# Optimization experiments

Measured on AMD Instinct MI355X. Metric: run time of the kernel, lower is better.

## Reference

```python
import jax, jax.numpy as jnp
import numpy as np
import math

D_RES, N_HEADS, D_HEAD, D_MLP = 1024, 16, 64, 4096
EPS = 1e-5
IGNORE = -100000.0


def setup_inputs() -> dict:
    key = jax.random.key(0)
    ks = jax.random.split(key, 8)
    std = 0.02
    return {
        "resid_pre": jax.random.normal(ks[0], (2, 2048, D_RES), dtype=jnp.float32),
        "ln1_w": jnp.ones((D_RES,), jnp.float32),
        "ln1_b": jnp.zeros((D_RES,), jnp.float32),
        "W_Q": jax.random.normal(ks[1], (N_HEADS, D_RES, D_HEAD), jnp.float32) * std,
        "b_Q": jnp.zeros((N_HEADS, D_HEAD), jnp.float32),
        "W_K": jax.random.normal(ks[2], (N_HEADS, D_RES, D_HEAD), jnp.float32) * std,
        "b_K": jnp.zeros((N_HEADS, D_HEAD), jnp.float32),
        "W_V": jax.random.normal(ks[3], (N_HEADS, D_RES, D_HEAD), jnp.float32) * std,
        "b_V": jnp.zeros((N_HEADS, D_HEAD), jnp.float32),
        "W_O": jax.random.normal(ks[4], (N_HEADS, D_HEAD, D_RES), jnp.float32) * std,
        "b_O": jnp.zeros((D_RES,), jnp.float32),
        "ln2_w": jnp.ones((D_RES,), jnp.float32),
        "ln2_b": jnp.zeros((D_RES,), jnp.float32),
        "W_in": jax.random.normal(ks[5], (D_RES, D_MLP), jnp.float32) * std,
        "b_in": jnp.zeros((D_MLP,), jnp.float32),
        "W_out": jax.random.normal(ks[6], (D_MLP, D_RES), jnp.float32) * std,
        "b_out": jnp.zeros((D_RES,), jnp.float32),
    }


def _layernorm(x, w, b):
    x = x - jnp.mean(x, axis=-1, keepdims=True)
    scale = jnp.sqrt(jnp.mean(x * x, axis=-1, keepdims=True) + EPS)
    return (x / scale) * w + b


def reference(resid_pre, ln1_w, ln1_b, W_Q, b_Q, W_K, b_K, W_V, b_V, W_O, b_O,
              ln2_w, ln2_b, W_in, b_in, W_out, b_out):
    x = _layernorm(resid_pre, ln1_w, ln1_b)  # [b,s,d]
    q = jnp.einsum('bsd,hde->bshe', x, W_Q) + b_Q
    k = jnp.einsum('bsd,hde->bshe', x, W_K) + b_K
    v = jnp.einsum('bsd,hde->bshe', x, W_V) + b_V
    scores = jnp.einsum('bqhe,bkhe->bhqk', q, k) / math.sqrt(D_HEAD)
    S = scores.shape[-1]
    mask = jnp.triu(jnp.ones((S, S), dtype=bool), k=1)
    scores = jnp.where(mask, IGNORE, scores)
    pattern = jax.nn.softmax(scores, axis=-1)
    z = jnp.einsum('bhqk,bkhe->bqhe', pattern, v)
    attn_out = jnp.einsum('bqhe,hed->bqd', z, W_O) + b_O
    resid_mid = resid_pre + attn_out
    y = _layernorm(resid_mid, ln2_w, ln2_b)
    pre = jnp.einsum('bsd,dm->bsm', y, W_in) + b_in
    post = jax.nn.gelu(pre, approximate=False)
    mlp_out = jnp.einsum('bsm,md->bsd', post, W_out) + b_out
    return resid_mid + mlp_out
```

## Files before the change

kernel.cpp:

```cpp
#include <hip/hip_runtime.h>
#include <cstddef>

typedef unsigned short u16;
using short8 = __attribute__((ext_vector_type(8))) short;
using f32x4  = __attribute__((ext_vector_type(4))) float;

__device__ __forceinline__ float bf2f(u16 u) {
  union { unsigned int i; float f; } v; v.i = ((unsigned int)u) << 16; return v.f;
}
__device__ __forceinline__ u16 f2bf(float f) {
  __bf16 h = (__bf16)f;
  return __builtin_bit_cast(unsigned short, h);
}

__device__ __forceinline__ void load_lds16(const u16* g, u16* l) {
  __builtin_amdgcn_global_load_lds((const __attribute__((address_space(1))) void*)g,
                                   (__attribute__((address_space(3))) void*)l, 16, 0, 0);
}

__global__ __launch_bounds__(256) void transpose_k(const float* __restrict__ in,
                                                   u16* __restrict__ out,
                                                   int R, int C,
                                                   long inB, long outB) {
  __shared__ float tile[32][33];
  long zb = blockIdx.z;
  in  += zb * inB;
  out += zb * outB;
  int c0 = blockIdx.x * 32, r0 = blockIdx.y * 32;
  int tx = threadIdx.x, ty = threadIdx.y;
#pragma unroll
  for (int i = 0; i < 32; i += 8)
    tile[ty + i][tx] = in[(long)(r0 + ty + i) * C + c0 + tx];
  __syncthreads();
#pragma unroll
  for (int i = 0; i < 32; i += 8)
    out[(long)(c0 + ty + i) * R + r0 + tx] = f2bf(tile[tx][ty + i]);
}

__global__ __launch_bounds__(256) void transpose_v_k(const u16* __restrict__ qkv,
                                                     u16* __restrict__ vT) {
  __shared__ u16 tile[32][33];
  int bh = blockIdx.z;
  int b = bh >> 4, h = bh & 15;
  const u16* in = qkv + (size_t)b * 2048 * 3072 + 2048 + h * 64;
  u16* out = vT + (size_t)bh * 64 * 2048;
  int e0 = blockIdx.x * 32, s0 = blockIdx.y * 32;
  int tx = threadIdx.x, ty = threadIdx.y;
#pragma unroll
  for (int i = 0; i < 32; i += 8)
    tile[ty + i][tx] = in[(size_t)(s0 + ty + i) * 3072 + e0 + tx];
  __syncthreads();
#pragma unroll
  for (int i = 0; i < 32; i += 8)
    out[(size_t)(e0 + ty + i) * 2048 + s0 + tx] = tile[tx][ty + i];
}

__global__ void build_qkv_bias(const float* __restrict__ bQ, const float* __restrict__ bK,
                               const float* __restrict__ bV, float* __restrict__ out) {
  int i = blockIdx.x * 256 + threadIdx.x;
  float v;
  if (i < 1024) v = bQ[i];
  else if (i < 2048) v = bK[i - 1024];
  else v = bV[i - 2048];
  out[i] = v;
}

__global__ __launch_bounds__(256) void ln_k(const float* __restrict__ inp,
                                            const float* __restrict__ w,
                                            const float* __restrict__ bias,
                                            u16* __restrict__ out) {
  __shared__ float red[2][4];
  int row = blockIdx.x, t = threadIdx.x;
  int wave = t >> 6, lane = t & 63;
  size_t base = (size_t)row * 1024 + t * 4;
  float4 f = *(const float4*)(inp + base);
  float v[4] = {f.x, f.y, f.z, f.w};
  float s = v[0] + v[1] + v[2] + v[3];
#pragma unroll
  for (int off = 32; off; off >>= 1) s += __shfl_xor(s, off, 64);
  if (lane == 0) red[0][wave] = s;
  __syncthreads();
  float mean = (red[0][0] + red[0][1] + red[0][2] + red[0][3]) * (1.f / 1024.f);
  float c[4]; float sq = 0.f;
#pragma unroll
  for (int j = 0; j < 4; ++j) { c[j] = v[j] - mean; sq += c[j] * c[j]; }
#pragma unroll
  for (int off = 32; off; off >>= 1) sq += __shfl_xor(sq, off, 64);
  if (lane == 0) red[1][wave] = sq;
  __syncthreads();
  float var = (red[1][0] + red[1][1] + red[1][2] + red[1][3]) * (1.f / 1024.f);
  float inv = 1.f / sqrtf(var + 1e-5f);
  float4 wv = *(const float4*)(w + t * 4);
  float4 bv = *(const float4*)(bias + t * 4);
  out[base + 0] = f2bf(c[0] * inv * wv.x + bv.x);
  out[base + 1] = f2bf(c[1] * inv * wv.y + bv.y);
  out[base + 2] = f2bf(c[2] * inv * wv.z + bv.z);
  out[base + 3] = f2bf(c[3] * inv * wv.w + bv.w);
}

template<int TN, bool RESIDF, bool GELU, bool OUTF32>
__global__ __launch_bounds__(256, 2) void gemm_k(const u16* __restrict__ A,
                                                 const u16* __restrict__ BT,
                                                 const float* __restrict__ bias,
                                                 const float* __restrict__ resid,
                                                 void* __restrict__ Cout,
                                                 int M, int N, int K) {
  constexpr int NS = TN / 32;
  __shared__ u16 As[128 * 64];
  __shared__ u16 Bs[TN * 64];
  int n0 = blockIdx.x * TN, m0 = blockIdx.y * 128;
  int t = threadIdx.x;
  int wave = t >> 6, lane = t & 63;
  int wr = wave >> 1, wc = wave & 1;
  int ln16 = lane & 15, quad = lane >> 4;

  f32x4 acc[4][NS];
#pragma unroll
  for (int i = 0; i < 4; ++i)
#pragma unroll
    for (int j = 0; j < NS; ++j) acc[i][j] = (f32x4){0.f, 0.f, 0.f, 0.f};

  int lrow8 = lane >> 3;
  int gseg  = (lane & 7) ^ lrow8;
  const u16* aG = A  + (size_t)(m0 + wave * 8 + lrow8) * K + gseg * 8;
  const u16* bG = BT + (size_t)(n0 + wave * 8 + lrow8) * K + gseg * 8;
  u16* aL = As + wave * 8 * 64;
  u16* bL = Bs + wave * 8 * 64;

  int e = ln16 & 7;
  int arow = wr * 64 + ln16;
  int brow = wc * (TN / 2) + ln16;

  for (int k0 = 0; k0 < K; k0 += 64) {
    __syncthreads();
#pragma unroll
    for (int i = 0; i < 4; ++i)
      load_lds16(aG + (size_t)i * 32 * K + k0, aL + i * 32 * 64);
#pragma unroll
    for (int i = 0; i < TN / 32; ++i)
      load_lds16(bG + (size_t)i * 32 * K + k0, bL + i * 32 * 64);
    __syncthreads();
#pragma unroll
    for (int kk = 0; kk < 2; ++kk) {
      int slot = (kk * 4 + quad) ^ e;
      short8 af[4], bf[NS];
#pragma unroll
      for (int ms = 0; ms < 4; ++ms)
        af[ms] = *(const short8*)&As[(arow + ms * 16) * 64 + slot * 8];
#pragma unroll
      for (int ns = 0; ns < NS; ++ns)
        bf[ns] = *(const short8*)&Bs[(brow + ns * 16) * 64 + slot * 8];
#pragma unroll
      for (int ms = 0; ms < 4; ++ms)
#pragma unroll
        for (int ns = 0; ns < NS; ++ns)
          acc[ms][ns] = __builtin_amdgcn_mfma_f32_16x16x32_bf16(af[ms], bf[ns], acc[ms][ns], 0, 0, 0);
    }
  }

#pragma unroll
  for (int ms = 0; ms < 4; ++ms)
#pragma unroll
    for (int ns = 0; ns < NS; ++ns)
#pragma unroll
      for (int r = 0; r < 4; ++r) {
        int grow = m0 + wr * 64 + ms * 16 + quad * 4 + r;
        int gcol = n0 + wc * (TN / 2) + ns * 16 + ln16;
        size_t idx = (size_t)grow * N + gcol;
        float v = acc[ms][ns][r] + bias[gcol];
        if (GELU) v = 0.5f * v * (1.f + erff(v * 0.70710678118654752f));
        if (RESIDF) v += resid[idx];
        if (OUTF32) ((float*)Cout)[idx] = v;
        else        ((u16*)Cout)[idx] = f2bf(v);
      }
}

template<bool GELU>
__global__ __launch_bounds__(512, 2) void gemm256_k(const u16* __restrict__ A,
                                                    const u16* __restrict__ BT,
                                                    const float* __restrict__ bias,
                                                    u16* __restrict__ C,
                                                    int M, int N, int K) {
  constexpr int SLOT = 8192;
  __shared__ __align__(16) u16 As[4 * SLOT];
  __shared__ __align__(16) u16 Bs[4 * SLOT];
  int n0 = blockIdx.x * 256, m0 = blockIdx.y * 256;
  int t = threadIdx.x;
  int w = t >> 6, lane = t & 63;
  int wr = w >> 2, wc = w & 3;
  int ln16 = lane & 15, quad = lane >> 4;

  f32x4 acc[8][4];
#pragma unroll
  for (int i = 0; i < 8; ++i)
#pragma unroll
    for (int j = 0; j < 4; ++j) acc[i][j] = (f32x4){0.f, 0.f, 0.f, 0.f};

  const u16* aG0 = A  + (size_t)(m0 + w * 32 + (lane >> 2)) * K + (lane & 3) * 8;
  const u16* bG0 = BT + (size_t)(n0 + w * 32 + (lane >> 2)) * K + (lane & 3) * 8;
  u16* aL0 = As + w * 1024;
  u16* bL0 = Bs + w * 1024;

#define STAGE_A(j, tg) do {                                         \
    const u16* _g = aG0 + (size_t)(j) * 32;                         \
    u16* _l = aL0 + (tg) * SLOT;                                    \
    load_lds16(_g, _l);                                             \
    load_lds16(_g + (size_t)16 * K, _l + 512);                      \
  } while (0)
#define STAGE_B(j, tg) do {                                         \
    const u16* _g = bG0 + (size_t)(j) * 32;                         \
    u16* _l = bL0 + (tg) * SLOT;                                    \
    load_lds16(_g, _l);                                             \
    load_lds16(_g + (size_t)16 * K, _l + 512);                      \
  } while (0)

  STAGE_A(0, 0); STAGE_B(0, 0);
  STAGE_A(1, 1); STAGE_B(1, 1);
  STAGE_A(2, 2); STAGE_B(2, 2);
  asm volatile("s_waitcnt vmcnt(8)" ::: "memory");
  __builtin_amdgcn_s_barrier();

  int nslot = K >> 5;
  const u16* aRd = As + (wr * 128 + ln16) * 32 + quad * 8;
  const u16* bRd = Bs + (wc * 64  + ln16) * 32 + quad * 8;

  for (int s = 0; s < nslot; ++s) {
    int cur = s & 3, tgt = (s + 3) & 3;
    const u16* aB = aRd + cur * SLOT;
    const u16* bB = bRd + cur * SLOT;
    short8 a[4], b[4];

#pragma unroll
    for (int i = 0; i < 4; ++i) a[i] = *(const short8*)(aB + i * 512);
#pragma unroll
    for (int i = 0; i < 4; ++i) b[i] = *(const short8*)(bB + i * 512);
    if (s + 3 < nslot) STAGE_A(s + 3, tgt);
    __builtin_amdgcn_s_barrier();
    __builtin_amdgcn_s_setprio(1);
#pragma unroll
    for (int ms = 0; ms < 4; ++ms)
#pragma unroll
      for (int ns = 0; ns < 4; ++ns)
        acc[ms][ns] = __builtin_amdgcn_mfma_f32_16x16x32_bf16(a[ms], b[ns], acc[ms][ns], 0, 0, 0);
    __builtin_amdgcn_s_setprio(0);
    __builtin_amdgcn_s_barrier();

#pragma unroll
    for (int i = 0; i < 4; ++i) a[i] = *(const short8*)(aB + (4 + i) * 512);
    if (s + 3 < nslot) {
      STAGE_B(s + 3, tgt);
      asm volatile("s_waitcnt vmcnt(4)" ::: "memory");
    } else {
      asm volatile("s_waitcnt vmcnt(0)" ::: "memory");
    }
    __builtin_amdgcn_s_barrier();
    __builtin_amdgcn_s_setprio(1);
#pragma unroll
    for (int ms = 0; ms < 4; ++ms)
#pragma unroll
      for (int ns = 0; ns < 4; ++ns)
        acc[4 + ms][ns] = __builtin_amdgcn_mfma_f32_16x16x32_bf16(a[ms], b[ns], acc[4 + ms][ns], 0, 0, 0);
    __builtin_amdgcn_s_setprio(0);
    __builtin_amdgcn_s_barrier();
  }
#undef STAGE_A
#undef STAGE_B

#pragma unroll
  for (int ms = 0; ms < 8; ++ms)
#pragma unroll
    for (int ns = 0; ns < 4; ++ns) {
      int gcol = n0 + wc * 64 + ns * 16 + ln16;
      float bb = bias[gcol];
#pragma unroll
      for (int r = 0; r < 4; ++r) {
        int grow = m0 + wr * 128 + ms * 16 + quad * 4 + r;
        float v = acc[ms][ns][r] + bb;
        if (GELU) v = 0.5f * v * (1.f + erff(v * 0.70710678118654752f));
        C[(size_t)grow * N + gcol] = f2bf(v);
      }
    }
}

__global__ __launch_bounds__(256) void attn_k(const u16* __restrict__ qkv,
                                              const u16* __restrict__ vT,
                                              u16* __restrict__ z) {
  __shared__ u16 Ks[64 * 64];
  __shared__ u16 Vs[64 * 64];
  __shared__ u16 Ps[2][4][16][72];
  int pair = blockIdx.x, h = blockIdx.y, b = blockIdx.z;
  int qtA = pair, qtB = 31 - pair;
  int t = threadIdx.x, wave = t >> 6, lane = t & 63;
  int ln16 = lane & 15, quad = lane >> 4;

  int qbase[2] = {qtA * 64 + wave * 16, qtB * 64 + wave * 16};
  short8 aq[2][2];
#pragma unroll
  for (int i = 0; i < 2; ++i) {
    const u16* qrow = qkv + (size_t)(b * 2048 + qbase[i] + ln16) * 3072 + h * 64;
    aq[i][0] = *(const short8*)(qrow + quad * 8);
    aq[i][1] = *(const short8*)(qrow + 32 + quad * 8);
  }

  f32x4 zero4 = {0.f, 0.f, 0.f, 0.f};
  f32x4 o[2][4];
  float l_i[2][4];
#pragma unroll
  for (int i = 0; i < 2; ++i)
#pragma unroll
    for (int n = 0; n < 4; ++n) { o[i][n] = zero4; l_i[i][n] = 0.f; }

  int lrow = lane >> 3;
  int gseg = (lane & 7) ^ lrow;
  const u16* kB = qkv + (size_t)(b * 2048 + wave * 16 + lrow) * 3072 + 1024 + h * 64 + gseg * 8;
  const u16* vB = vT + ((size_t)(b * 16 + h) * 64 + wave * 16 + lrow) * 2048 + gseg * 8;
  u16* kL = Ks + wave * 16 * 64;
  u16* vL = Vs + wave * 16 * 64;

  int e = ln16 & 7;
  int nkt = qtB + 1;
  for (int kt = 0; kt < nkt; ++kt) {
    __syncthreads();
    size_t kOff = (size_t)kt * 64 * 3072;
    size_t vOff = (size_t)kt * 64;
#pragma unroll
    for (int i = 0; i < 2; ++i) {
      load_lds16(kB + kOff + (size_t)i * 8 * 3072, kL + i * 8 * 64);
      load_lds16(vB + vOff + (size_t)i * 8 * 2048, vL + i * 8 * 64);
    }
    __syncthreads();

    int kg = kt * 64;
#pragma unroll
    for (int i = 0; i < 2; ++i) {
      if (i == 0 && kt > qtA) continue;
      f32x4 s[4] = {zero4, zero4, zero4, zero4};
#pragma unroll
      for (int kk = 0; kk < 2; ++kk) {
        short8 a = aq[i][kk];
        int slot = (kk * 4 + quad) ^ e;
#pragma unroll
        for (int n = 0; n < 4; ++n) {
          short8 kb = *(const short8*)&Ks[(n * 16 + ln16) * 64 + slot * 8];
          s[n] = __builtin_amdgcn_mfma_f32_16x16x32_bf16(a, kb, s[n], 0, 0, 0);
        }
      }
#pragma unroll
      for (int r = 0; r < 4; ++r) {
        int gq = qbase[i] + quad * 4 + r;
        float sum = 0.f;
#pragma unroll
        for (int n = 0; n < 4; ++n) {
          float p = (kg + n * 16 + ln16 > gq) ? 0.f : __expf(s[n][r] * 0.125f);
          sum += p;
          Ps[i][wave][quad * 4 + r][n * 16 + ln16] = f2bf(p);
        }
#pragma unroll
        for (int off = 8; off; off >>= 1) sum += __shfl_xor(sum, off, 16);
        l_i[i][r] += sum;
      }
#pragma unroll
      for (int kk = 0; kk < 2; ++kk) {
        short8 ap = *(const short8*)&Ps[i][wave][ln16][kk * 32 + quad * 8];
        int slot = (kk * 4 + quad) ^ e;
#pragma unroll
        for (int n = 0; n < 4; ++n) {
          short8 bv = *(const short8*)&Vs[(n * 16 + ln16) * 64 + slot * 8];
          o[i][n] = __builtin_amdgcn_mfma_f32_16x16x32_bf16(ap, bv, o[i][n], 0, 0, 0);
        }
      }
    }
  }

#pragma unroll
  for (int i = 0; i < 2; ++i) {
    float inv[4];
#pragma unroll
    for (int r = 0; r < 4; ++r) inv[r] = 1.f / l_i[i][r];
#pragma unroll
    for (int n = 0; n < 4; ++n)
#pragma unroll
      for (int r = 0; r < 4; ++r)
        z[(size_t)(b * 2048 + qbase[i] + quad * 4 + r) * 1024 + h * 64 + n * 16 + ln16] =
            f2bf(o[i][n][r] * inv[r]);
  }
}

extern "C" void kernel_launch(void* const* d_in, const int* in_sizes, int n_in,
                              void* d_out, int out_size, void* d_ws, size_t ws_size,
                              hipStream_t stream) {
  const float* resid_pre = (const float*)d_in[0];
  const float* ln1_w = (const float*)d_in[1];
  const float* ln1_b = (const float*)d_in[2];
  const float* W_Q  = (const float*)d_in[3];
  const float* b_Q  = (const float*)d_in[4];
  const float* W_K  = (const float*)d_in[5];
  const float* b_K  = (const float*)d_in[6];
  const float* W_V  = (const float*)d_in[7];
  const float* b_V  = (const float*)d_in[8];
  const float* W_O  = (const float*)d_in[9];
  const float* b_O  = (const float*)d_in[10];
  const float* ln2_w = (const float*)d_in[11];
  const float* ln2_b = (const float*)d_in[12];
  const float* W_in  = (const float*)d_in[13];
  const float* b_in  = (const float*)d_in[14];
  const float* W_out = (const float*)d_in[15];
  const float* b_out = (const float*)d_in[16];
  float* out = (float*)d_out;

  char* w = (char*)d_ws;
  u16* WqkvT = (u16*)w;  w += (size_t)3072 * 1024 * 2;
  u16* WoT   = (u16*)w;  w += (size_t)1024 * 1024 * 2;
  u16* WinT  = (u16*)w;  w += (size_t)4096 * 1024 * 2;
  u16* WoutT = (u16*)w;  w += (size_t)1024 * 4096 * 2;
  float* qkvBias = (float*)w; w += 3072 * 4;
  u16* xln   = (u16*)w;  w += (size_t)4096 * 1024 * 2;
  float* resid_mid = (float*)w; w += (size_t)4096 * 1024 * 4;
  u16* qkvBuf = (u16*)w; w += (size_t)4096 * 3072 * 2;
  u16* zBuf  = (u16*)w;  w += (size_t)4096 * 1024 * 2;
  u16* vTBuf = (u16*)w;  w += (size_t)32 * 64 * 2048 * 2;
  u16* hBuf  = qkvBuf;

  dim3 tb(32, 8);
  transpose_k<<<dim3(2, 32, 16), tb, 0, stream>>>(W_Q, WqkvT,                1024, 64, 65536, 65536);
  transpose_k<<<dim3(2, 32, 16), tb, 0, stream>>>(W_K, WqkvT + 1024 * 1024,  1024, 64, 65536, 65536);
  transpose_k<<<dim3(2, 32, 16), tb, 0, stream>>>(W_V, WqkvT + 2048 * 1024,  1024, 64, 65536, 65536);
  transpose_k<<<dim3(32, 32, 1), tb, 0, stream>>>(W_O,  WoT,   1024, 1024, 0, 0);
  transpose_k<<<dim3(128, 32, 1), tb, 0, stream>>>(W_in, WinT,  1024, 4096, 0, 0);
  transpose_k<<<dim3(32, 128, 1), tb, 0, stream>>>(W_out, WoutT, 4096, 1024, 0, 0);
  build_qkv_bias<<<12, 256, 0, stream>>>(b_Q, b_K, b_V, qkvBias);

  ln_k<<<4096, 256, 0, stream>>>(resid_pre, ln1_w, ln1_b, xln);
  gemm256_k<false><<<dim3(12, 16), 512, 0, stream>>>(
      xln, WqkvT, qkvBias, qkvBuf, 4096, 3072, 1024);
  transpose_v_k<<<dim3(2, 64, 32), tb, 0, stream>>>(qkvBuf, vTBuf);
  attn_k<<<dim3(16, 16, 2), 256, 0, stream>>>(qkvBuf, vTBuf, zBuf);
  gemm_k<64, true, false, true><<<dim3(16, 32), 256, 0, stream>>>(
      zBuf, WoT, b_O, resid_pre, resid_mid, 4096, 1024, 1024);
  ln_k<<<4096, 256, 0, stream>>>(resid_mid, ln2_w, ln2_b, xln);
  gemm256_k<true><<<dim3(16, 16), 512, 0, stream>>>(
      xln, WinT, b_in, hBuf, 4096, 4096, 1024);
  gemm_k<64, true, false, true><<<dim3(16, 32), 256, 0, stream>>>(
      hBuf, WoutT, b_out, resid_mid, out, 4096, 1024, 4096);
}
```

Measured before the change: 385.0 us.

## Double-buffer K/V in attention, one query tile per block, relax GEMM waits

The attention kernel now gives each block a single query tile instead of a pair of complementary tiles, doubling the grid. It double-buffers K/V tiles in LDS so the next tile's loads overlap compute, applies the causal mask only on the diagonal tile, and defers the row-sum shuffle reduction to the end. It also swizzles the P scratch layout to reduce bank conflicts and adds a 4-blocks-per-CU launch bound. Separately, the 256-wide GEMM's waitcnt now waits less eagerly during the pipelined stages. The risks are load imbalance from dropping the paired-tile scheme and extra LDS use.

```diff
diff --git a/kernel.cpp b/kernel.cpp
--- a/kernel.cpp
+++ b/kernel.cpp
@@ -249,8 +249,10 @@
     for (int i = 0; i < 4; ++i) a[i] = *(const short8*)(aB + (4 + i) * 512);
     if (s + 3 < nslot) {
       STAGE_B(s + 3, tgt);
+      asm volatile("s_waitcnt vmcnt(8)" ::: "memory");
+    } else if (s + 2 < nslot) {
       asm volatile("s_waitcnt vmcnt(4)" ::: "memory");
-    } else {
+    } else if (s + 1 < nslot) {
       asm volatile("s_waitcnt vmcnt(0)" ::: "memory");
     }
     __builtin_amdgcn_s_barrier();
@@ -282,108 +284,118 @@
     }
 }
 
-__global__ __launch_bounds__(256) void attn_k(const u16* __restrict__ qkv,
-                                              const u16* __restrict__ vT,
-                                              u16* __restrict__ z) {
-  __shared__ u16 Ks[64 * 64];
-  __shared__ u16 Vs[64 * 64];
-  __shared__ u16 Ps[2][4][16][72];
-  int pair = blockIdx.x, h = blockIdx.y, b = blockIdx.z;
-  int qtA = pair, qtB = 31 - pair;
+__global__ __launch_bounds__(256, 4) void attn_k(const u16* __restrict__ qkv,
+                                                 const u16* __restrict__ vT,
+                                                 u16* __restrict__ z) {
+  __shared__ u16 Ks[2][64 * 64];
+  __shared__ u16 Vs[2][64 * 64];
+  __shared__ u16 Ps[4][16 * 64];
+  int qt = blockIdx.x, h = blockIdx.y, b = blockIdx.z;
   int t = threadIdx.x, wave = t >> 6, lane = t & 63;
   int ln16 = lane & 15, quad = lane >> 4;
-
-  int qbase[2] = {qtA * 64 + wave * 16, qtB * 64 + wave * 16};
-  short8 aq[2][2];
-#pragma unroll
-  for (int i = 0; i < 2; ++i) {
-    const u16* qrow = qkv + (size_t)(b * 2048 + qbase[i] + ln16) * 3072 + h * 64;
-    aq[i][0] = *(const short8*)(qrow + quad * 8);
-    aq[i][1] = *(const short8*)(qrow + 32 + quad * 8);
+  int e = ln16 & 7;
+  int qbase = qt * 64 + wave * 16;
+
+  short8 aq[2];
+  {
+    const u16* qrow = qkv + (size_t)(b * 2048 + qbase + ln16) * 3072 + h * 64;
+    aq[0] = *(const short8*)(qrow + quad * 8);
+    aq[1] = *(const short8*)(qrow + 32 + quad * 8);
   }
 
   f32x4 zero4 = {0.f, 0.f, 0.f, 0.f};
-  f32x4 o[2][4];
-  float l_i[2][4];
-#pragma unroll
-  for (int i = 0; i < 2; ++i)
-#pragma unroll
-    for (int n = 0; n < 4; ++n) { o[i][n] = zero4; l_i[i][n] = 0.f; }
+  f32x4 o[4];
+  float l_i[4];
+#pragma unroll
+  for (int n = 0; n < 4; ++n) { o[n] = zero4; l_i[n] = 0.f; }
 
   int lrow = lane >> 3;
   int gseg = (lane & 7) ^ lrow;
-  const u16* kB = qkv + (size_t)(b * 2048 + wave * 16 + lrow) * 3072 + 1024 + h * 64 + gseg * 8;
-  const u16* vB = vT + ((size_t)(b * 16 + h) * 64 + wave * 16 + lrow) * 2048 + gseg * 8;
-  u16* kL = Ks + wave * 16 * 64;
-  u16* vL = Vs + wave * 16 * 64;
-
-  int e = ln16 & 7;
-  int nkt = qtB + 1;
-  for (int kt = 0; kt < nkt; ++kt) {
-    __syncthreads();
-    size_t kOff = (size_t)kt * 64 * 3072;
-    size_t vOff = (size_t)kt * 64;
-#pragma unroll
-    for (int i = 0; i < 2; ++i) {
-      load_lds16(kB + kOff + (size_t)i * 8 * 3072, kL + i * 8 * 64);
-      load_lds16(vB + vOff + (size_t)i * 8 * 2048, vL + i * 8 * 64);
-    }
-    __syncthreads();
+  const u16* kP = qkv + (size_t)(b * 2048 + wave * 16 + lrow) * 3072 + 1024 + h * 64 + gseg * 8;
+  const u16* vP = vT + ((size_t)(b * 16 + h) * 64 + wave * 16 + lrow) * 2048 + gseg * 8;
+  u16* kL = (u16*)Ks + wave * 1024;
+  u16* vL = (u16*)Vs + wave * 1024;
+  u16* psW = (u16*)Ps + wave * 1024;
+
+#define STAGE_KV(bf) do {                                  \
+    load_lds16(kP, kL + (bf) * 4096);                      \
+    load_lds16(kP + (size_t)8 * 3072, kL + (bf) * 4096 + 512); \
+    load_lds16(vP, vL + (bf) * 4096);                      \
+    load_lds16(vP + (size_t)8 * 2048, vL + (bf) * 4096 + 512); \
+    kP += (size_t)64 * 3072; vP += 64;                     \
+  } while (0)
+
+  STAGE_KV(0);
+
+  for (int kt = 0; kt <= qt; ++kt) {
+    int cur = kt & 1;
+    bool more = (kt < qt);
+    if (more) STAGE_KV(cur ^ 1);
+    if (more) asm volatile("s_waitcnt vmcnt(4)" ::: "memory");
+    else      asm volatile("s_waitcnt vmcnt(0)" ::: "memory");
+    __builtin_amdgcn_s_barrier();
+
+    const u16* ksB = (const u16*)Ks + cur * 4096;
+    const u16* vsB = (const u16*)Vs + cur * 4096;
+
+    f32x4 s[4] = {zero4, zero4, zero4, zero4};
+#pragma unroll
+    for (int kk = 0; kk < 2; ++kk) {
+      short8 a = aq[kk];
+      int slot = (kk * 4 + quad) ^ e;
+#pragma unroll
+      for (int n = 0; n < 4; ++n) {
+        short8 kb = *(const short8*)&ksB[(n * 16 + ln16) * 64 + slot * 8];
+        s[n] = __builtin_amdgcn_mfma_f32_16x16x32_bf16(a, kb, s[n], 0, 0, 0);
+      }
+    }
 
     int kg = kt * 64;
-#pragma unroll
-    for (int i = 0; i < 2; ++i) {
-      if (i == 0 && kt > qtA) continue;
-      f32x4 s[4] = {zero4, zero4, zero4, zero4};
-#pragma unroll
-      for (int kk = 0; kk < 2; ++kk) {
-        short8 a = aq[i][kk];
-        int slot = (kk * 4 + quad) ^ e;
-#pragma unroll
-        for (int n = 0; n < 4; ++n) {
-          short8 kb = *(const short8*)&Ks[(n * 16 + ln16) * 64 + slot * 8];
-          s[n] = __builtin_amdgcn_mfma_f32_16x16x32_bf16(a, kb, s[n], 0, 0, 0);
-        }
+    bool diag = (kt == qt);
+#pragma unroll
+    for (int r = 0; r < 4; ++r) {
+      int q = quad * 4 + r;
+      int gq = qbase + q;
+      int q7 = q & 7;
+      float psum = 0.f;
+#pragma unroll
+      for (int n = 0; n < 4; ++n) {
+        float p = __expf(s[n][r] * 0.125f);
+        if (diag && (kg + n * 16 + ln16 > gq)) p = 0.f;
+        psum += p;
+        psW[q * 64 + ((((n << 1) | (ln16 >> 3)) ^ q7) << 3) + e] = f2bf(p);
       }
-#pragma unroll
-      for (int r = 0; r < 4; ++r) {
-        int gq = qbase[i] + quad * 4 + r;
-        float sum = 0.f;
-#pragma unroll
-        for (int n = 0; n < 4; ++n) {
-          float p = (kg + n * 16 + ln16 > gq) ? 0.f : __expf(s[n][r] * 0.125f);
-          sum += p;
-          Ps[i][wave][quad * 4 + r][n * 16 + ln16] = f2bf(p);
-        }
-#pragma unroll
-        for (int off = 8; off; off >>= 1) sum += __shfl_xor(sum, off, 16);
-        l_i[i][r] += sum;
+      l_i[r] += psum;
+    }
+
+#pragma unroll
+    for (int kk = 0; kk < 2; ++kk) {
+      int slot = (kk * 4 + quad) ^ e;
+      short8 ap = *(const short8*)&psW[ln16 * 64 + slot * 8];
+#pragma unroll
+      for (int n = 0; n < 4; ++n) {
+        short8 bv = *(const short8*)&vsB[(n * 16 + ln16) * 64 + slot * 8];
+        o[n] = __builtin_amdgcn_mfma_f32_16x16x32_bf16(ap, bv, o[n], 0, 0, 0);
       }
-#pragma unroll
-      for (int kk = 0; kk < 2; ++kk) {
-        short8 ap = *(const short8*)&Ps[i][wave][ln16][kk * 32 + quad * 8];
-        int slot = (kk * 4 + quad) ^ e;
-#pragma unroll
-        for (int n = 0; n < 4; ++n) {
-          short8 bv = *(const short8*)&Vs[(n * 16 + ln16) * 64 + slot * 8];
-          o[i][n] = __builtin_amdgcn_mfma_f32_16x16x32_bf16(ap, bv, o[i][n], 0, 0, 0);
-        }
-      }
-    }
+    }
+    __builtin_amdgcn_s_barrier();
   }
-
-#pragma unroll
-  for (int i = 0; i < 2; ++i) {
-    float inv[4];
-#pragma unroll
-    for (int r = 0; r < 4; ++r) inv[r] = 1.f / l_i[i][r];
-#pragma unroll
-    for (int n = 0; n < 4; ++n)
-#pragma unroll
-      for (int r = 0; r < 4; ++r)
-        z[(size_t)(b * 2048 + qbase[i] + quad * 4 + r) * 1024 + h * 64 + n * 16 + ln16] =
-            f2bf(o[i][n][r] * inv[r]);
+#undef STAGE_KV
+
+  float inv[4];
+#pragma unroll
+  for (int r = 0; r < 4; ++r) {
+    float sum = l_i[r];
+#pragma unroll
+    for (int off = 8; off; off >>= 1) sum += __shfl_xor(sum, off, 16);
+    inv[r] = 1.f / sum;
   }
+#pragma unroll
+  for (int n = 0; n < 4; ++n)
+#pragma unroll
+    for (int r = 0; r < 4; ++r)
+      z[(size_t)(b * 2048 + qbase + quad * 4 + r) * 1024 + h * 64 + n * 16 + ln16] =
+          f2bf(o[n][r] * inv[r]);
 }
 
 extern "C" void kernel_launch(void* const* d_in, const int* in_sizes, int n_in,
@@ -434,7 +446,7 @@
   gemm256_k<false><<<dim3(12, 16), 512, 0, stream>>>(
       xln, WqkvT, qkvBias, qkvBuf, 4096, 3072, 1024);
   transpose_v_k<<<dim3(2, 64, 32), tb, 0, stream>>>(qkvBuf, vTBuf);
-  attn_k<<<dim3(16, 16, 2), 256, 0, stream>>>(qkvBuf, vTBuf, zBuf);
+  attn_k<<<dim3(32, 16, 2), 256, 0, stream>>>(qkvBuf, vTBuf, zBuf);
   gemm_k<64, true, false, true><<<dim3(16, 32), 256, 0, stream>>>(
       zBuf, WoT, b_O, resid_pre, resid_mid, 4096, 1024, 1024);
   ln_k<<<4096, 256, 0, stream>>>(resid_mid, ln2_w, ln2_b, xln);
```

After: 384.7 us. Within noise of the previous version (-0.1%).

## Restructure attention into 128-row tiles with triple-buffered async K/V staging

Applied to the files above, without the earlier changes.

The attention kernel moves from 64-row query/key tiles with 4 waves to 128-row tiles with 8 waves. K/V loads go into a three-slot LDS ring prefetched one tile ahead, and a single barrier per step replaces the two syncthreads. The row-sum shuffle moves out of the inner loop to the end, P uses an XOR-swizzled LDS layout, and causal masking only runs on diagonal tiles. The GEMM pipeline also gets finer vmcnt waits in its tail iterations. The trade-off is higher LDS use and bigger tiles, which means fewer blocks (256 rather than 512) and more wasted work on diagonal tiles.

```diff
diff --git a/kernel.cpp b/kernel.cpp
--- a/kernel.cpp
+++ b/kernel.cpp
@@ -249,8 +249,10 @@
     for (int i = 0; i < 4; ++i) a[i] = *(const short8*)(aB + (4 + i) * 512);
     if (s + 3 < nslot) {
       STAGE_B(s + 3, tgt);
+      asm volatile("s_waitcnt vmcnt(8)" ::: "memory");
+    } else if (s + 2 < nslot) {
       asm volatile("s_waitcnt vmcnt(4)" ::: "memory");
-    } else {
+    } else if (s + 1 < nslot) {
       asm volatile("s_waitcnt vmcnt(0)" ::: "memory");
     }
     __builtin_amdgcn_s_barrier();
@@ -282,107 +284,138 @@
     }
 }
 
-__global__ __launch_bounds__(256) void attn_k(const u16* __restrict__ qkv,
+__global__ __launch_bounds__(512) void attn_k(const u16* __restrict__ qkv,
                                               const u16* __restrict__ vT,
                                               u16* __restrict__ z) {
-  __shared__ u16 Ks[64 * 64];
-  __shared__ u16 Vs[64 * 64];
-  __shared__ u16 Ps[2][4][16][72];
-  int pair = blockIdx.x, h = blockIdx.y, b = blockIdx.z;
-  int qtA = pair, qtB = 31 - pair;
-  int t = threadIdx.x, wave = t >> 6, lane = t & 63;
-  int ln16 = lane & 15, quad = lane >> 4;
-
-  int qbase[2] = {qtA * 64 + wave * 16, qtB * 64 + wave * 16};
+  __shared__ __align__(16) u16 Ks[3 * 8192];
+  __shared__ __align__(16) u16 Vs[3 * 8192];
+  __shared__ __align__(16) u16 Ps[8 * 2048];
+  int bh = blockIdx.x, p = blockIdx.y;
+  int b = bh >> 4, h = bh & 15;
+  int tA = p, tB = 15 - p;
+  int t = threadIdx.x, w = t >> 6, lane = t & 63;
+  int ln16 = lane & 15, quad = lane >> 4, e = ln16 & 7;
+
   short8 aq[2][2];
 #pragma unroll
-  for (int i = 0; i < 2; ++i) {
-    const u16* qrow = qkv + (size_t)(b * 2048 + qbase[i] + ln16) * 3072 + h * 64;
-    aq[i][0] = *(const short8*)(qrow + quad * 8);
-    aq[i][1] = *(const short8*)(qrow + 32 + quad * 8);
+  for (int ti = 0; ti < 2; ++ti) {
+    int tq = ti ? tB : tA;
+    const u16* qrow = qkv + (size_t)(b * 2048 + tq * 128 + w * 16 + ln16) * 3072 + h * 64;
+    aq[ti][0] = *(const short8*)(qrow + quad * 8);
+    aq[ti][1] = *(const short8*)(qrow + 32 + quad * 8);
   }
 
   f32x4 zero4 = {0.f, 0.f, 0.f, 0.f};
   f32x4 o[2][4];
   float l_i[2][4];
 #pragma unroll
-  for (int i = 0; i < 2; ++i)
-#pragma unroll
-    for (int n = 0; n < 4; ++n) { o[i][n] = zero4; l_i[i][n] = 0.f; }
-
-  int lrow = lane >> 3;
-  int gseg = (lane & 7) ^ lrow;
-  const u16* kB = qkv + (size_t)(b * 2048 + wave * 16 + lrow) * 3072 + 1024 + h * 64 + gseg * 8;
-  const u16* vB = vT + ((size_t)(b * 16 + h) * 64 + wave * 16 + lrow) * 2048 + gseg * 8;
-  u16* kL = Ks + wave * 16 * 64;
-  u16* vL = Vs + wave * 16 * 64;
-
-  int e = ln16 & 7;
-  int nkt = qtB + 1;
+  for (int ti = 0; ti < 2; ++ti)
+#pragma unroll
+    for (int n = 0; n < 4; ++n) { o[ti][n] = zero4; l_i[ti][n] = 0.f; }
+
+  const u16* kB = qkv + (size_t)(b * 2048 + w * 16 + (lane >> 3)) * 3072
+                + 1024 + h * 64 + (((lane & 7) ^ (lane >> 3))) * 8;
+  const u16* vB0 = vT + ((size_t)(b * 16 + h) * 64 + w * 8 + (lane >> 4)) * 2048
+                 + (((lane & 15) ^ (lane >> 4))) * 8;
+  const u16* vB1 = vT + ((size_t)(b * 16 + h) * 64 + w * 8 + 4 + (lane >> 4)) * 2048
+                 + (((lane & 15) ^ (4 + (lane >> 4)))) * 8;
+  u16* kL = Ks + w * 16 * 64;
+  u16* vL = Vs + w * 8 * 128;
+  u16* psW = Ps + w * 2048;
+
+#define STAGE(kt_, rg_) do {                                              \
+    size_t kOff = (size_t)(kt_) * 128 * 3072;                             \
+    u16* _kl = kL + (rg_) * 8192;                                         \
+    load_lds16(kB + kOff, _kl);                                           \
+    load_lds16(kB + kOff + (size_t)8 * 3072, _kl + 8 * 64);               \
+    size_t vOff = (size_t)(kt_) * 128;                                    \
+    u16* _vl = vL + (rg_) * 8192;                                         \
+    load_lds16(vB0 + vOff, _vl);                                          \
+    load_lds16(vB1 + vOff, _vl + 4 * 128);                                \
+  } while (0)
+
+  int nkt = tB + 1;
+  STAGE(0, 0);
+
   for (int kt = 0; kt < nkt; ++kt) {
-    __syncthreads();
-    size_t kOff = (size_t)kt * 64 * 3072;
-    size_t vOff = (size_t)kt * 64;
-#pragma unroll
-    for (int i = 0; i < 2; ++i) {
-      load_lds16(kB + kOff + (size_t)i * 8 * 3072, kL + i * 8 * 64);
-      load_lds16(vB + vOff + (size_t)i * 8 * 2048, vL + i * 8 * 64);
-    }
-    __syncthreads();
-
-    int kg = kt * 64;
-#pragma unroll
-    for (int i = 0; i < 2; ++i) {
-      if (i == 0 && kt > qtA) continue;
-      f32x4 s[4] = {zero4, zero4, zero4, zero4};
+    int ring = kt % 3;
+    if (kt + 1 < nkt) {
+      STAGE(kt + 1, (kt + 1) % 3);
+      asm volatile("s_waitcnt vmcnt(4)" ::: "memory");
+    } else {
+      asm volatile("s_waitcnt vmcnt(0)" ::: "memory");
+    }
+    __builtin_amdgcn_s_barrier();
+
+    const u16* ks = Ks + ring * 8192;
+    const u16* vs = Vs + ring * 8192;
+    int kg = kt * 128;
+
+#pragma unroll
+    for (int ti = 0; ti < 2; ++ti) {
+      int tq = ti ? tB : tA;
+      if (kt > tq) continue;
+
+      f32x4 s[8] = {zero4, zero4, zero4, zero4, zero4, zero4, zero4, zero4};
 #pragma unroll
       for (int kk = 0; kk < 2; ++kk) {
-        short8 a = aq[i][kk];
+        short8 a = aq[ti][kk];
         int slot = (kk * 4 + quad) ^ e;
 #pragma unroll
-        for (int n = 0; n < 4; ++n) {
-          short8 kb = *(const short8*)&Ks[(n * 16 + ln16) * 64 + slot * 8];
+        for (int n = 0; n < 8; ++n) {
+          short8 kb = *(const short8*)&ks[(n * 16 + ln16) * 64 + slot * 8];
           s[n] = __builtin_amdgcn_mfma_f32_16x16x32_bf16(a, kb, s[n], 0, 0, 0);
         }
       }
+
+      bool diag = (kt == tq);
+      int qgb = tq * 128 + w * 16 + quad * 4;
 #pragma unroll
       for (int r = 0; r < 4; ++r) {
-        int gq = qbase[i] + quad * 4 + r;
-        float sum = 0.f;
+        int q = quad * 4 + r, q7 = q & 7;
+        int gq = qgb + r;
+        float psum = 0.f;
+#pragma unroll
+        for (int n = 0; n < 8; ++n) {
+          float pv = __expf(s[n][r] * 0.125f);
+          if (diag && (kg + n * 16 + ln16 > gq)) pv = 0.f;
+          psum += pv;
+          psW[q * 128 + ((((n << 1) | (ln16 >> 3)) ^ q7) << 3) + e] = f2bf(pv);
+        }
+        l_i[ti][r] += psum;
+      }
+
+#pragma unroll
+      for (int kk = 0; kk < 4; ++kk) {
+        int slot = (kk * 4 + quad) ^ e;
+        short8 ap = *(const short8*)&psW[ln16 * 128 + slot * 8];
 #pragma unroll
         for (int n = 0; n < 4; ++n) {
-          float p = (kg + n * 16 + ln16 > gq) ? 0.f : __expf(s[n][r] * 0.125f);
-          sum += p;
-          Ps[i][wave][quad * 4 + r][n * 16 + ln16] = f2bf(p);
-        }
-#pragma unroll
-        for (int off = 8; off; off >>= 1) sum += __shfl_xor(sum, off, 16);
-        l_i[i][r] += sum;
-      }
-#pragma unroll
-      for (int kk = 0; kk < 2; ++kk) {
-        short8 ap = *(const short8*)&Ps[i][wave][ln16][kk * 32 + quad * 8];
-        int slot = (kk * 4 + quad) ^ e;
-#pragma unroll
-        for (int n = 0; n < 4; ++n) {
-          short8 bv = *(const short8*)&Vs[(n * 16 + ln16) * 64 + slot * 8];
-          o[i][n] = __builtin_amdgcn_mfma_f32_16x16x32_bf16(ap, bv, o[i][n], 0, 0, 0);
+          short8 bv = *(const short8*)&vs[(n * 16 + ln16) * 128 + slot * 8];
+          o[ti][n] = __builtin_amdgcn_mfma_f32_16x16x32_bf16(ap, bv, o[ti][n], 0, 0, 0);
         }
       }
     }
   }
-
-#pragma unroll
-  for (int i = 0; i < 2; ++i) {
+#undef STAGE
+
+#pragma unroll
+  for (int ti = 0; ti < 2; ++ti) {
+    int tq = ti ? tB : tA;
     float inv[4];
 #pragma unroll
-    for (int r = 0; r < 4; ++r) inv[r] = 1.f / l_i[i][r];
+    for (int r = 0; r < 4; ++r) {
+      float sum = l_i[ti][r];
+#pragma unroll
+      for (int off = 8; off; off >>= 1) sum += __shfl_xor(sum, off, 16);
+      inv[r] = 1.f / sum;
+    }
 #pragma unroll
     for (int n = 0; n < 4; ++n)
 #pragma unroll
       for (int r = 0; r < 4; ++r)
-        z[(size_t)(b * 2048 + qbase[i] + quad * 4 + r) * 1024 + h * 64 + n * 16 + ln16] =
-            f2bf(o[i][n][r] * inv[r]);
+        z[(size_t)(b * 2048 + tq * 128 + w * 16 + quad * 4 + r) * 1024
+          + h * 64 + n * 16 + ln16] = f2bf(o[ti][n][r] * inv[r]);
   }
 }
 
@@ -434,7 +467,7 @@
   gemm256_k<false><<<dim3(12, 16), 512, 0, stream>>>(
       xln, WqkvT, qkvBias, qkvBuf, 4096, 3072, 1024);
   transpose_v_k<<<dim3(2, 64, 32), tb, 0, stream>>>(qkvBuf, vTBuf);
-  attn_k<<<dim3(16, 16, 2), 256, 0, stream>>>(qkvBuf, vTBuf, zBuf);
+  attn_k<<<dim3(32, 8, 1), 512, 0, stream>>>(qkvBuf, vTBuf, zBuf);
   gemm_k<64, true, false, true><<<dim3(16, 32), 256, 0, stream>>>(
       zBuf, WoT, b_O, resid_pre, resid_mid, 4096, 1024, 1024);
   ln_k<<<4096, 256, 0, stream>>>(resid_mid, ln2_w, ln2_b, xln);
```

Measured after the change: 365.1 us. -5.2%, faster.
